# Optimization experiments

Hardware: AMD Instinct MI355X
Metric: run time of the kernel (lower is better)

Reference implementation:

```python
import jax, jax.numpy as jnp
import numpy as np

B, S, D = 2, 2048, 768
H = 12
DEPTH = D // H
DFF = 4 * D
EPS = 1e-5


def setup_inputs() -> dict:
    key = jax.random.key(0)
    ks = jax.random.split(key, 9)
    sd = 0.02
    return {
        "x": jax.random.normal(ks[0], (B, S, D), dtype=jnp.float32),
        "Wqkv": jax.random.normal(ks[1], (D, 3 * D), dtype=jnp.float32) * sd,
        "Wout": jax.random.normal(ks[2], (D, D), dtype=jnp.float32) * sd,
        "bout": jnp.zeros((D,), dtype=jnp.float32),
        "W1": jax.random.normal(ks[3], (D, DFF), dtype=jnp.float32) * sd,
        "b1": jnp.zeros((DFF,), dtype=jnp.float32),
        "W2": jax.random.normal(ks[4], (DFF, D), dtype=jnp.float32) * sd,
        "b2": jnp.zeros((D,), dtype=jnp.float32),
        "g1": jnp.ones((D,), dtype=jnp.float32),
        "be1": jnp.zeros((D,), dtype=jnp.float32),
        "g2": jnp.ones((D,), dtype=jnp.float32),
        "be2": jnp.zeros((D,), dtype=jnp.float32),
    }


def _layernorm(x, gain, bias):
    mean = jnp.mean(x, axis=-1, keepdims=True)
    var = jnp.mean(jnp.square(x - mean), axis=-1, keepdims=True)  # unbiased=False
    return gain * (x - mean) / jnp.sqrt(var + EPS) + bias


def reference(x, Wqkv, Wout, bout, W1, b1, W2, b2, g1, be1, g2, be2):
    b, s, d = x.shape
    # QKV projection (no bias), chunk into q,k,v
    qkv = jnp.einsum("bsd,de->bse", x, Wqkv)
    q, k, v = jnp.split(qkv, 3, axis=-1)
    q = q.reshape(b, s, H, DEPTH).transpose(0, 2, 1, 3)  # bhsd
    k = k.reshape(b, s, H, DEPTH).transpose(0, 2, 1, 3)
    v = v.reshape(b, s, H, DEPTH).transpose(0, 2, 1, 3)
    scores = jnp.einsum("bhqd,bhkd->bhqk", q, k) / np.sqrt(DEPTH).astype(np.float32)
    # causal mask (use_masking=True)
    causal = jnp.tril(jnp.ones((s, s), dtype=bool))
    scores = jnp.where(causal, scores, -jnp.inf)
    attn = jax.nn.softmax(scores, axis=-1)
    ctx = jnp.einsum("bhqk,bhkd->bhqd", attn, v)
    ctx = ctx.transpose(0, 2, 1, 3).reshape(b, s, d)
    attn_out = jnp.einsum("bsd,de->bse", ctx, Wout) + bout
    # residual + LN1 (dropout is identity in eval)
    h = _layernorm(x + attn_out, g1, be1)
    # FFN
    ff = jax.nn.relu(jnp.einsum("bsd,df->bsf", h, W1) + b1)
    ff = jnp.einsum("bsf,fd->bsd", ff, W2) + b2
    return _layernorm(h + ff, g2, be2)
```

## Files before the change

### kernel.cpp

```cpp
#include <hip/hip_runtime.h>


typedef __attribute__((ext_vector_type(8))) short  short8;
typedef __attribute__((ext_vector_type(4))) float  floatx4;

#define QSC 0.18033688f
#define C2  24.0f

__device__ __forceinline__ float b2f(unsigned short u) {
    return __uint_as_float(((unsigned)u) << 16);
}
__device__ __forceinline__ unsigned short f2b(float f) {
    unsigned x = __float_as_uint(f);
    return (unsigned short)((x + 0x7fffu + ((x >> 16) & 1u)) >> 16);
}
__device__ __forceinline__ void async_cp16(const void* g, void* l) {
    __builtin_amdgcn_global_load_lds((const __attribute__((address_space(1))) void*)g,
                                     (__attribute__((address_space(3))) void*)l,
                                     16, 0, 0);
}
__device__ __forceinline__ int chunk_ofs(int qb) {
    int t = qb >> 1;
    return (qb & 1) ? (t + 1) * (t + 1) : t * (t + 1);
}
__device__ __forceinline__ int swz16(int row, int chunk) {
    return row * 64 + (((chunk ^ (row & 7)) & 7) << 3);
}

__global__ __launch_bounds__(256) void prep_all(
    const float* __restrict__ x,    unsigned short* __restrict__ xb,
    const float* __restrict__ Wqkv, unsigned short* __restrict__ wqkvT,
    const float* __restrict__ Wout, unsigned short* __restrict__ woutT,
    const float* __restrict__ W1,   unsigned short* __restrict__ w1T,
    const float* __restrict__ W2,   unsigned short* __restrict__ w2T)
{
    __shared__ float tile[32][33];
    int idx = blockIdx.x;
    int tx = threadIdx.x & 31, ty = threadIdx.x >> 5;
    if (idx >= 6912) {
        int i = (idx - 6912) * 256 + threadIdx.x;
        float4 v = ((const float4*)x)[i];
        ushort4 u;
        u.x = f2b(v.x); u.y = f2b(v.y); u.z = f2b(v.z); u.w = f2b(v.w);
        ((ushort4*)xb)[i] = u;
        return;
    }
    const float* W; unsigned short* Wt; int K, N, bx, by;
    if (idx < 1728)      { W = Wqkv; Wt = wqkvT; K = 768;  N = 2304; bx = idx % 72;        by = idx / 72; }
    else if (idx < 2304) { W = Wout; Wt = woutT; K = 768;  N = 768;  bx = (idx-1728) % 24; by = (idx-1728) / 24; }
    else if (idx < 4608) { W = W1;   Wt = w1T;   K = 768;  N = 3072; bx = (idx-2304) % 96; by = (idx-2304) / 96; }
    else                 { W = W2;   Wt = w2T;   K = 3072; N = 768;  bx = (idx-4608) % 24; by = (idx-4608) / 24; }
    int n0 = bx * 32, k0 = by * 32;
    for (int i = ty; i < 32; i += 8)
        tile[i][tx] = W[(size_t)(k0 + i) * N + n0 + tx];
    __syncthreads();
    for (int i = ty; i < 32; i += 8)
        Wt[(size_t)(n0 + i) * K + k0 + tx] = f2b(tile[tx][i]);
}

__global__ __launch_bounds__(256) void gemm_bf16(
    const unsigned short* __restrict__ A,
    const unsigned short* __restrict__ Bt,
    const float* __restrict__ bias,
    float* __restrict__ outF,
    unsigned short* __restrict__ outB,
    int M, int N, int K, int relu, int mode, int kslab)
{
    __shared__ unsigned short As[8192];
    __shared__ unsigned short Bs[8192];
    const int tid  = threadIdx.x;
    const int m0   = blockIdx.y * 128;
    const int n0   = blockIdx.x * 128;
    const int kz   = blockIdx.z;
    const int kbeg = kz * kslab;
    const int kend = kbeg + kslab;
    const int lane = tid & 63;
    const int wave = tid >> 6;
    const int wm   = (wave >> 1) * 64;
    const int wn   = (wave & 1) * 64;
    const int fr   = lane & 15;
    const int fq   = lane >> 4;

    floatx4 acc[4][4];
    for (int i = 0; i < 4; i++)
        for (int j = 0; j < 4; j++)
            for (int e = 0; e < 4; e++) acc[i][j][e] = 0.f;

    for (int kk = kbeg; kk < kend; kk += 64) {
        __syncthreads();
        #pragma unroll
        for (int r = 0; r < 4; ++r) {
            int c   = r * 256 + tid;
            int row = c >> 3;
            int jj  = ((c & 7) ^ (row & 7)) * 8;
            async_cp16(A  + (size_t)(m0 + row) * K + kk + jj, &As[c * 8]);
            async_cp16(Bt + (size_t)(n0 + row) * K + kk + jj, &Bs[c * 8]);
        }
        __syncthreads();

        #pragma unroll
        for (int kc = 0; kc < 2; ++kc) {
            short8 a[4], b[4];
            #pragma unroll
            for (int t = 0; t < 4; t++) a[t] = *(const short8*)&As[swz16(wm + t * 16 + fr, kc * 4 + fq)];
            #pragma unroll
            for (int t = 0; t < 4; t++) b[t] = *(const short8*)&Bs[swz16(wn + t * 16 + fr, kc * 4 + fq)];
            #pragma unroll
            for (int i = 0; i < 4; i++)
                #pragma unroll
                for (int j = 0; j < 4; j++)
                    acc[i][j] = __builtin_amdgcn_mfma_f32_16x16x32_bf16(a[i], b[j], acc[i][j], 0, 0, 0);
        }
    }

    if (mode == 2) {
        float* dst = outF + (size_t)kz * M * N;
        #pragma unroll
        for (int j = 0; j < 4; j++) {
            int col = n0 + wn + j * 16 + fr;
            #pragma unroll
            for (int i = 0; i < 4; i++) {
                int rbase = m0 + wm + i * 16 + fq * 4;
                #pragma unroll
                for (int e = 0; e < 4; e++)
                    dst[(size_t)(rbase + e) * N + col] = acc[i][j][e];
            }
        }
        return;
    }
    if (mode == 1) {
        #pragma unroll
        for (int j = 0; j < 4; j++) {
            int col   = n0 + wn + j * 16 + fr;
            int which = (col >= 1536) ? 2 : (col >= 768 ? 1 : 0);
            float sc  = (which == 0) ? QSC : 1.0f;
            int rem   = col - which * 768;
            int hh    = rem >> 6, d = rem & 63;
            #pragma unroll
            for (int i = 0; i < 4; i++) {
                int rbase = m0 + wm + i * 16 + fq * 4;
                #pragma unroll
                for (int e = 0; e < 4; e++) {
                    int row = rbase + e;
                    int b_  = row >> 11, srow = row & 2047;
                    size_t idx = (size_t)which * 3145728 +
                                 ((size_t)(b_ * 12 + hh) * 2048 + srow) * 64 + d;
                    outB[idx] = f2b(acc[i][j][e] * sc);
                }
            }
        }
        return;
    }
    #pragma unroll
    for (int j = 0; j < 4; j++) {
        int col  = n0 + wn + j * 16 + fr;
        float bv = bias ? bias[col] : 0.f;
        #pragma unroll
        for (int i = 0; i < 4; i++) {
            int rbase = m0 + wm + i * 16 + fq * 4;
            #pragma unroll
            for (int e = 0; e < 4; e++) {
                float v = acc[i][j][e] + bv;
                if (relu) v = fmaxf(v, 0.f);
                size_t idx = (size_t)(rbase + e) * N + col;
                if (outF) outF[idx] = v;
                if (outB) outB[idx] = f2b(v);
            }
        }
    }
}

__global__ __launch_bounds__(256) void attn_part(const unsigned short* __restrict__ Qg,
                                                 const unsigned short* __restrict__ Kg,
                                                 const unsigned short* __restrict__ Vg,
                                                 unsigned short* __restrict__ pO,
                                                 float* __restrict__ pL) {
    __shared__ unsigned short Ks[2][4096];
    __shared__ unsigned short Vt[2][4096];
    __shared__ unsigned short Ps[128 * 72];
    const int tid  = threadIdx.x;
    const int lane = tid & 63;
    const int wave = tid >> 6;
    const int fr   = lane & 15;
    const int fq   = lane >> 4;
    const int wm   = wave * 32;
    const int r    = 71 - blockIdx.x;
    const int bh   = blockIdx.y;
    int qb = 0;
    for (int q_ = 15; q_ >= 0; --q_) if (r >= chunk_ofs(q_)) { qb = q_; break; }
    const int c     = r - chunk_ofs(qb);
    const int q0    = qb * 128;
    const int tile0 = 4 * c;
    const int ntk   = min(4, 2 * (qb + 1) - 4 * c);
    const int slot  = bh * 72 + r;
    const unsigned short* Qb = Qg + (size_t)bh * 2048 * 64;
    const unsigned short* Kb = Kg + (size_t)bh * 2048 * 64;
    const unsigned short* Vb = Vg + (size_t)bh * 2048 * 64;

    short8 qf[2][2];
    #pragma unroll
    for (int rf = 0; rf < 2; ++rf) {
        const unsigned short* qr = Qb + (size_t)(q0 + wm + rf * 16 + fr) * 64;
        qf[rf][0] = *(const short8*)(qr + fq * 8);
        qf[rf][1] = *(const short8*)(qr + 32 + fq * 8);
    }

    short8 onesf;
    #pragma unroll
    for (int i = 0; i < 8; ++i) onesf[i] = (short)0x3F80;

    floatx4 o[2][4];
    floatx4 lacc[2];
    #pragma unroll
    for (int rf = 0; rf < 2; ++rf) {
        #pragma unroll
        for (int nt = 0; nt < 4; ++nt)
            #pragma unroll
            for (int e = 0; e < 4; ++e) o[rf][nt][e] = 0.f;
        #pragma unroll
        for (int e = 0; e < 4; ++e) lacc[rf][e] = 0.f;
    }

    const int c0 = tid, c1 = tid + 256;
    uint4 kr0, kr1, vr0, vr1;

#define LOADT(TG)                                                              \
    {                                                                          \
        int base = (TG) * 64;                                                  \
        kr0 = *(const uint4*)(Kb + (size_t)(base + (c0 >> 3)) * 64 + (c0 & 7) * 8); \
        kr1 = *(const uint4*)(Kb + (size_t)(base + (c1 >> 3)) * 64 + (c1 & 7) * 8); \
        vr0 = *(const uint4*)(Vb + (size_t)(base + (c0 & 63)) * 64 + (c0 >> 6) * 8); \
        vr1 = *(const uint4*)(Vb + (size_t)(base + (c1 & 63)) * 64 + (c1 >> 6) * 8); \
    }
#define WRITET(BUF)                                                            \
    {                                                                          \
        *(uint4*)&Ks[BUF][swz16(c0 >> 3, c0 & 7)] = kr0;                       \
        *(uint4*)&Ks[BUF][swz16(c1 >> 3, c1 & 7)] = kr1;                       \
        unsigned short t0[8]; *(uint4*)t0 = vr0;                               \
        _Pragma("unroll") for (int i_ = 0; i_ < 8; ++i_)                       \
            Vt[BUF][((c0 >> 6) * 8 + i_) * 64 +                                \
                    (((((c0 >> 3) & 7) ^ i_) << 3) | (c0 & 7))] = t0[i_];      \
        unsigned short t1[8]; *(uint4*)t1 = vr1;                               \
        _Pragma("unroll") for (int i_ = 0; i_ < 8; ++i_)                       \
            Vt[BUF][((c1 >> 6) * 8 + i_) * 64 +                                \
                    (((((c1 >> 3) & 7) ^ i_) << 3) | (c1 & 7))] = t1[i_];      \
    }

    LOADT(tile0);
    WRITET(0);
    __syncthreads();

    for (int kt = 0; kt < ntk; ++kt) {
        const int  tg   = tile0 + kt;
        const int  cur  = kt & 1;
        const bool more = (kt + 1 < ntk);
        if (more) LOADT(tg + 1);

        short8 kf[2][4];
        #pragma unroll
        for (int kc = 0; kc < 2; ++kc)
            #pragma unroll
            for (int nt = 0; nt < 4; ++nt)
                kf[kc][nt] = *(const short8*)&Ks[cur][swz16(nt * 16 + fr, kc * 4 + fq)];

        floatx4 s[2][4];
        #pragma unroll
        for (int rf = 0; rf < 2; ++rf)
            #pragma unroll
            for (int nt = 0; nt < 4; ++nt)
                #pragma unroll
                for (int e = 0; e < 4; ++e) s[rf][nt][e] = 0.f;
        #pragma unroll
        for (int rf = 0; rf < 2; ++rf)
            #pragma unroll
            for (int kc = 0; kc < 2; ++kc)
                #pragma unroll
                for (int nt = 0; nt < 4; ++nt)
                    s[rf][nt] = __builtin_amdgcn_mfma_f32_16x16x32_bf16(qf[rf][kc], kf[kc][nt], s[rf][nt], 0, 0, 0);

        const bool need_mask = (tg * 64 + 63) > (q0 + wm);
        #pragma unroll
        for (int rf = 0; rf < 2; ++rf) {
            const int rmin  = q0 + wm + rf * 16;
            const int pbase = (wm + rf * 16 + fq * 4) * 72 + fr;
            #pragma unroll
            for (int nt = 0; nt < 4; ++nt) {
                const bool tmask = need_mask && (tg * 64 + nt * 16 + 15 > rmin);
                const int  kvc   = tg * 64 + nt * 16 + fr;
                #pragma unroll
                for (int e = 0; e < 4; ++e) {
                    float v = s[rf][nt][e] - C2;
                    if (tmask && kvc > rmin + fq * 4 + e) v = -1e30f;
                    float pv = __builtin_amdgcn_exp2f(v);
                    Ps[pbase + e * 72 + nt * 16] =
                        (unsigned short)(__float_as_uint(pv) >> 16);
                }
            }
        }
        __asm__ volatile("s_waitcnt lgkmcnt(0)" ::: "memory");

        short8 pf[2][2], vf[2][4];
        #pragma unroll
        for (int rf = 0; rf < 2; ++rf)
            #pragma unroll
            for (int kc = 0; kc < 2; ++kc)
                pf[rf][kc] = *(const short8*)&Ps[(wm + rf * 16 + fr) * 72 + kc * 32 + fq * 8];
        #pragma unroll
        for (int kc = 0; kc < 2; ++kc)
            #pragma unroll
            for (int nt = 0; nt < 4; ++nt)
                vf[kc][nt] = *(const short8*)&Vt[cur][swz16(nt * 16 + fr, kc * 4 + fq)];
        #pragma unroll
        for (int rf = 0; rf < 2; ++rf)
            #pragma unroll
            for (int kc = 0; kc < 2; ++kc) {
                lacc[rf] = __builtin_amdgcn_mfma_f32_16x16x32_bf16(pf[rf][kc], onesf, lacc[rf], 0, 0, 0);
                #pragma unroll
                for (int nt = 0; nt < 4; ++nt)
                    o[rf][nt] = __builtin_amdgcn_mfma_f32_16x16x32_bf16(pf[rf][kc], vf[kc][nt], o[rf][nt], 0, 0, 0);
            }

        if (more) {
            WRITET(cur ^ 1);
            __syncthreads();
        }
    }
#undef LOADT
#undef WRITET

    #pragma unroll
    for (int rf = 0; rf < 2; ++rf)
        #pragma unroll
        for (int e = 0; e < 4; ++e) {
            int row = wm + rf * 16 + fq * 4 + e;
            unsigned short* orow = pO + ((size_t)slot * 128 + row) * 64;
            #pragma unroll
            for (int nt = 0; nt < 4; ++nt)
                orow[nt * 16 + fr] = f2b(o[rf][nt][e]);
            if (fr == 0)
                pL[(size_t)slot * 128 + row] = lacc[rf][e];
        }
}

__global__ __launch_bounds__(256) void attn_combine(const unsigned short* __restrict__ pO,
                                                    const float* __restrict__ pL,
                                                    unsigned short* __restrict__ ctx) {
    const int qb  = blockIdx.x;
    const int bh  = blockIdx.y;
    const int b   = bh / 12, h = bh % 12;
    const int nch = (qb + 2) >> 1;
    const int slot0 = bh * 72 + chunk_ofs(qb);
    const int tid = threadIdx.x;
    const int row = tid >> 1;
    const int col0 = (tid & 1) * 32;

    float L = 0.f;
    for (int i = 0; i < nch; ++i)
        L += pL[(size_t)(slot0 + i) * 128 + row];

    float acc[32];
    #pragma unroll
    for (int j = 0; j < 32; ++j) acc[j] = 0.f;
    for (int i = 0; i < nch; ++i) {
        const unsigned short* p = pO + ((size_t)(slot0 + i) * 128 + row) * 64 + col0;
        #pragma unroll
        for (int v4 = 0; v4 < 4; ++v4) {
            uint4 u = *(const uint4*)(p + v4 * 8);
            unsigned short t[8]; *(uint4*)t = u;
            #pragma unroll
            for (int j = 0; j < 8; ++j) acc[v4 * 8 + j] += b2f(t[j]);
        }
    }
    float inv = 1.f / L;
    unsigned short* orow = ctx + ((size_t)(b * 2048 + qb * 128 + row)) * 768 + h * 64 + col0;
    #pragma unroll
    for (int v4 = 0; v4 < 4; ++v4) {
        unsigned short t[8];
        #pragma unroll
        for (int j = 0; j < 8; ++j) t[j] = f2b(acc[v4 * 8 + j] * inv);
        *(uint4*)(orow + v4 * 8) = *(uint4*)t;
    }
}

__global__ __launch_bounds__(256) void resid_ln2(const float* __restrict__ X,
                                                 const float* __restrict__ P,
                                                 int nsplit,
                                                 const float* __restrict__ bv,
                                                 const float* __restrict__ gain,
                                                 const float* __restrict__ beta,
                                                 float* __restrict__ outF,
                                                 unsigned short* __restrict__ outB) {
    const int row = blockIdx.x;
    const int t   = threadIdx.x;
    const size_t off = (size_t)row * 768;
    float v[3];
    #pragma unroll
    for (int i = 0; i < 3; i++) {
        size_t c = off + t + i * 256;
        float r = X[c] + bv[t + i * 256];
        for (int p = 0; p < nsplit; ++p) r += P[(size_t)p * 3145728 + c];
        v[i] = r;
    }
    float s  = v[0] + v[1] + v[2];
    float s2 = v[0] * v[0] + v[1] * v[1] + v[2] * v[2];
    #pragma unroll
    for (int o2 = 32; o2 > 0; o2 >>= 1) {
        s  += __shfl_down(s,  o2);
        s2 += __shfl_down(s2, o2);
    }
    __shared__ float rs[4], rq[4];
    if ((t & 63) == 0) { rs[t >> 6] = s; rq[t >> 6] = s2; }
    __syncthreads();
    float S    = rs[0] + rs[1] + rs[2] + rs[3];
    float S2   = rq[0] + rq[1] + rq[2] + rq[3];
    float mean = S * (1.0f / 768.0f);
    float var  = S2 * (1.0f / 768.0f) - mean * mean;
    float inv  = rsqrtf(var + 1e-5f);
    #pragma unroll
    for (int i = 0; i < 3; i++) {
        int c   = t + i * 256;
        float y = gain[c] * (v[i] - mean) * inv + beta[c];
        if (outF) outF[off + c] = y;
        if (outB) outB[off + c] = f2b(y);
    }
}

extern "C" void kernel_launch(void* const* d_in, const int* in_sizes, int n_in,
                              void* d_out, int out_size, void* d_ws, size_t ws_size,
                              hipStream_t stream) {
    const float* x    = (const float*)d_in[0];
    const float* Wqkv = (const float*)d_in[1];
    const float* Wout = (const float*)d_in[2];
    const float* bout = (const float*)d_in[3];
    const float* W1   = (const float*)d_in[4];
    const float* b1   = (const float*)d_in[5];
    const float* W2   = (const float*)d_in[6];
    const float* b2   = (const float*)d_in[7];
    const float* g1   = (const float*)d_in[8];
    const float* be1  = (const float*)d_in[9];
    const float* g2   = (const float*)d_in[10];
    const float* be2  = (const float*)d_in[11];
    float* out = (float*)d_out;

    char* ws = (char*)d_ws;
    unsigned short* wqkvT  = (unsigned short*)(ws + 0);
    unsigned short* woutT  = (unsigned short*)(ws + 3538944);
    unsigned short* w1T    = (unsigned short*)(ws + 4718592);
    unsigned short* w2T    = (unsigned short*)(ws + 9437184);
    unsigned short* xb     = (unsigned short*)(ws + 14155776);
    unsigned short* qkvG   = (unsigned short*)(ws + 20447232);
    unsigned short* Qg     = qkvG;
    unsigned short* Kg     = qkvG + 3145728;
    unsigned short* Vg     = qkvG + 6291456;
    unsigned short* pO     = (unsigned short*)(ws + 39321600);
    float*          pL     = (float*)(ws + 67633152);
    unsigned short* ctxb   = (unsigned short*)(ws + 14155776);
    float*          WoutP  = (float*)(ws + 39321600);
    float*          h      = (float*)(ws + 20447232);
    unsigned short* hb     = (unsigned short*)(ws + 77070336);
    unsigned short* ffb    = (unsigned short*)(ws + 39321600);
    float*          W2P    = (float*)(ws + 64487424);

    prep_all<<<9984, 256, 0, stream>>>(x, xb, Wqkv, wqkvT, Wout, woutT, W1, w1T, W2, w2T);
    gemm_bf16<<<dim3(18, 32), 256, 0, stream>>>(xb, wqkvT, nullptr, nullptr, qkvG,
                                                4096, 2304, 768, 0, 1, 768);
    attn_part<<<dim3(72, 24), 256, 0, stream>>>(Qg, Kg, Vg, pO, pL);
    attn_combine<<<dim3(16, 24), 256, 0, stream>>>(pO, pL, ctxb);
    gemm_bf16<<<dim3(6, 32, 3), 256, 0, stream>>>(ctxb, woutT, nullptr, WoutP, nullptr,
                                                  4096, 768, 768, 0, 2, 256);
    resid_ln2<<<4096, 256, 0, stream>>>(x, WoutP, 3, bout, g1, be1, h, hb);
    gemm_bf16<<<dim3(24, 32), 256, 0, stream>>>(hb, w1T, b1, nullptr, ffb,
                                                4096, 3072, 768, 1, 0, 768);
    gemm_bf16<<<dim3(6, 32, 2), 256, 0, stream>>>(ffb, w2T, nullptr, W2P, nullptr,
                                                  4096, 768, 3072, 0, 2, 1536);
    resid_ln2<<<4096, 256, 0, stream>>>(h, W2P, 2, b2, g2, be2, out, nullptr);
}
```

Before: 310.8 us.

## Double-buffer GEMM LDS tiles with BK=32 to overlap loads and MFMA

Replaces the single 128x128x64 LDS stage in the bf16 GEMM with two 128x128x32 buffers. The next K-slice is prefetched asynchronously into the alternate buffer while MFMAs run on the current one, so there is one barrier per iteration instead of two. This aims to hide global-to-LDS latency behind compute. The trade-off is a smaller K step, which means more iterations and barriers per unit of work, and a new 4-chunk swizzle that may raise LDS bank conflicts.

After: 324.0 us. +4.2%, slower.

```diff
diff --git a/kernel.cpp b/kernel.cpp
--- a/kernel.cpp
+++ b/kernel.cpp
@@ -25,6 +25,9 @@
 }
 __device__ __forceinline__ int swz16(int row, int chunk) {
     return row * 64 + (((chunk ^ (row & 7)) & 7) << 3);
+}
+__device__ __forceinline__ int swz32(int row, int chunk) {
+    return row * 32 + (((chunk ^ row) & 3) << 3);
 }
 
 __global__ __launch_bounds__(256) void prep_all(
@@ -66,52 +69,60 @@
     unsigned short* __restrict__ outB,
     int M, int N, int K, int relu, int mode, int kslab)
 {
-    __shared__ unsigned short As[8192];
-    __shared__ unsigned short Bs[8192];
+    __shared__ unsigned short As[2][4096];
+    __shared__ unsigned short Bs[2][4096];
     const int tid  = threadIdx.x;
     const int m0   = blockIdx.y * 128;
     const int n0   = blockIdx.x * 128;
     const int kz   = blockIdx.z;
     const int kbeg = kz * kslab;
-    const int kend = kbeg + kslab;
     const int lane = tid & 63;
     const int wave = tid >> 6;
     const int wm   = (wave >> 1) * 64;
     const int wn   = (wave & 1) * 64;
     const int fr   = lane & 15;
     const int fq   = lane >> 4;
+    const int nIt  = kslab >> 5;
 
     floatx4 acc[4][4];
     for (int i = 0; i < 4; i++)
         for (int j = 0; j < 4; j++)
             for (int e = 0; e < 4; e++) acc[i][j][e] = 0.f;
 
-    for (int kk = kbeg; kk < kend; kk += 64) {
+#define STAGE(KK, BUF)                                                         \
+    {                                                                          \
+        _Pragma("unroll") for (int r_ = 0; r_ < 2; ++r_) {                     \
+            int c_   = r_ * 256 + tid;                                         \
+            int row_ = c_ >> 2;                                                \
+            int jj_  = (((c_ & 3) ^ (row_ & 3)) << 3);                         \
+            async_cp16(A  + (size_t)(m0 + row_) * K + (KK) + jj_,              \
+                       &As[BUF][c_ * 8]);                                      \
+            async_cp16(Bt + (size_t)(n0 + row_) * K + (KK) + jj_,              \
+                       &Bs[BUF][c_ * 8]);                                      \
+        }                                                                      \
+    }
+
+    STAGE(kbeg, 0);
+    __syncthreads();
+
+    for (int it = 0; it < nIt; ++it) {
+        const int cur = it & 1;
+        if (it + 1 < nIt) STAGE(kbeg + (it + 1) * 32, cur ^ 1);
+
+        short8 a[4], b[4];
+        #pragma unroll
+        for (int t = 0; t < 4; t++) a[t] = *(const short8*)&As[cur][swz32(wm + t * 16 + fr, fq)];
+        #pragma unroll
+        for (int t = 0; t < 4; t++) b[t] = *(const short8*)&Bs[cur][swz32(wn + t * 16 + fr, fq)];
+        #pragma unroll
+        for (int i = 0; i < 4; i++)
+            #pragma unroll
+            for (int j = 0; j < 4; j++)
+                acc[i][j] = __builtin_amdgcn_mfma_f32_16x16x32_bf16(a[i], b[j], acc[i][j], 0, 0, 0);
+
         __syncthreads();
-        #pragma unroll
-        for (int r = 0; r < 4; ++r) {
-            int c   = r * 256 + tid;
-            int row = c >> 3;
-            int jj  = ((c & 7) ^ (row & 7)) * 8;
-            async_cp16(A  + (size_t)(m0 + row) * K + kk + jj, &As[c * 8]);
-            async_cp16(Bt + (size_t)(n0 + row) * K + kk + jj, &Bs[c * 8]);
-        }
-        __syncthreads();
-
-        #pragma unroll
-        for (int kc = 0; kc < 2; ++kc) {
-            short8 a[4], b[4];
-            #pragma unroll
-            for (int t = 0; t < 4; t++) a[t] = *(const short8*)&As[swz16(wm + t * 16 + fr, kc * 4 + fq)];
-            #pragma unroll
-            for (int t = 0; t < 4; t++) b[t] = *(const short8*)&Bs[swz16(wn + t * 16 + fr, kc * 4 + fq)];
-            #pragma unroll
-            for (int i = 0; i < 4; i++)
-                #pragma unroll
-                for (int j = 0; j < 4; j++)
-                    acc[i][j] = __builtin_amdgcn_mfma_f32_16x16x32_bf16(a[i], b[j], acc[i][j], 0, 0, 0);
-        }
-    }
+    }
+#undef STAGE
 
     if (mode == 2) {
         float* dst = outF + (size_t)kz * M * N;
```
